# Performance work log

Measured on AMD Instinct MI355X. Metric: run time of the kernel, lower is better.

The kernel has to match this reference:

```python
import jax, jax.numpy as jnp
import numpy as np


def binarize_weight(w):
    # clip to [-1,1], sign in forward, straight-through gradient of clip in backward
    clipped = jnp.clip(w, -1.0, 1.0)
    rounded = jnp.sign(clipped)
    return clipped + jax.lax.stop_gradient(rounded - clipped)


def setup_inputs() -> dict:
    key = jax.random.key(0)
    k1, k2 = jax.random.split(key)
    d_in, filters = 4096, 4096
    n_tokens = 8192
    stdv = 1.0 / np.sqrt(d_in)
    x = jax.random.normal(k1, (n_tokens, d_in), dtype=jnp.float32)
    w = jax.random.normal(k2, (d_in, filters), dtype=jnp.float32) * stdv
    b = jnp.zeros((filters,), dtype=jnp.float32)
    return {"x": x, "w": w, "b": b}


def reference(x, w, b):
    # [N, d_in] @ binarized [d_in, filters] + bias
    out = jnp.matmul(x, binarize_weight(w))
    return out + b
```

## Files before the change

kernel.cpp:

```cpp
#include <hip/hip_runtime.h>
#include <hip/hip_bf16.h>
#include <cstdint>

typedef __attribute__((ext_vector_type(8))) short bf16x8;
typedef __attribute__((ext_vector_type(4))) float f32x4;
typedef __attribute__((ext_vector_type(4))) int   i32x4;
typedef __attribute__((ext_vector_type(16))) int  i32x16;

static constexpr int Mdim = 8192;
static constexpr int Kdim = 4096;
static constexpr int Ndim = 4096;
static constexpr int BM = 256, BN = 256;
static constexpr int BKB = 128;
static constexpr int NKT = Kdim / BKB;

static constexpr int QBLOCKS = Mdim / 4;
static constexpr int SBLOCKS = (Kdim / 64) * (Ndim / 64);

__device__ __forceinline__ void async_copy16(const void* g, void* l) {
  __builtin_amdgcn_global_load_lds(
      (const __attribute__((address_space(1))) void*)g,
      (__attribute__((address_space(3))) void*)l, 16, 0, 0);
}

__global__ __launch_bounds__(256) void prep_kernel(const float* __restrict__ x,
                                                   int8_t* __restrict__ xq,
                                                   float* __restrict__ srow,
                                                   const float* __restrict__ w,
                                                   int8_t* __restrict__ wsT) {
  const int tid = threadIdx.x;
  if (blockIdx.x < QBLOCKS) {
    const int wv  = tid >> 6;
    const int l   = tid & 63;
    const int row = blockIdx.x * 4 + wv;
    const float* xr = x + (size_t)row * Kdim;
    float4 v[16];
    float m = 0.f;
    #pragma unroll
    for (int j = 0; j < 16; ++j) {
      v[j] = *reinterpret_cast<const float4*>(xr + (size_t)(j * 64 + l) * 4);
      m = fmaxf(m, fmaxf(fmaxf(fabsf(v[j].x), fabsf(v[j].y)),
                         fmaxf(fabsf(v[j].z), fabsf(v[j].w))));
    }
    #pragma unroll
    for (int s = 32; s >= 1; s >>= 1) m = fmaxf(m, __shfl_xor(m, s, 64));
    const float rs = (m > 0.f) ? (127.0f / m) : 0.f;
    if (l == 0) srow[row] = m * (1.0f / 127.0f);
    uint32_t* xq32 = reinterpret_cast<uint32_t*>(xq + (size_t)row * Kdim);
    #pragma unroll
    for (int j = 0; j < 16; ++j) {
      int a0 = (int)rintf(v[j].x * rs), a1 = (int)rintf(v[j].y * rs);
      int a2 = (int)rintf(v[j].z * rs), a3 = (int)rintf(v[j].w * rs);
      uint32_t p = (uint32_t)(a0 & 255) | ((uint32_t)(a1 & 255) << 8) |
                   ((uint32_t)(a2 & 255) << 16) | ((uint32_t)(a3 & 255) << 24);
      xq32[j * 64 + l] = p;
    }
  } else {
    __shared__ int8_t t[64 * 68];
    const int bid = blockIdx.x - QBLOCKS;
    const int k0 = (bid & 63) * 64;
    const int n0 = (bid >> 6) * 64;
    #pragma unroll
    for (int r = 0; r < 4; ++r) {
      int c  = r * 256 + tid;
      int k  = c >> 4;
      int n4 = (c & 15) * 4;
      float4 v = *reinterpret_cast<const float4*>(w + (size_t)(k0 + k) * Ndim + n0 + n4);
      int s0 = (v.x > 0.f) - (v.x < 0.f);
      int s1 = (v.y > 0.f) - (v.y < 0.f);
      int s2 = (v.z > 0.f) - (v.z < 0.f);
      int s3 = (v.w > 0.f) - (v.w < 0.f);
      uint32_t p = (uint32_t)(s0 & 255) | ((uint32_t)(s1 & 255) << 8) |
                   ((uint32_t)(s2 & 255) << 16) | ((uint32_t)(s3 & 255) << 24);
      *reinterpret_cast<uint32_t*>(&t[k * 68 + n4]) = p;
    }
    __syncthreads();
    const int n  = tid & 63;
    const int ck = (tid >> 6) * 16;
    union { int8_t b[16]; uint4 u; } o;
    #pragma unroll
    for (int j = 0; j < 16; ++j) o.b[j] = t[(ck + j) * 68 + n];
    *reinterpret_cast<uint4*>(wsT + (size_t)(n0 + n) * Kdim + k0 + ck) = o.u;
  }
}

__global__ __launch_bounds__(512, 2) void gemm_i8_kernel(const int8_t* __restrict__ A,
                                                         const int8_t* __restrict__ Bt,
                                                         const float* __restrict__ srow,
                                                         const float* __restrict__ bias,
                                                         float* __restrict__ out) {
  __shared__ int8_t sA[2][BM * BKB];
  __shared__ int8_t sB[2][BN * BKB];
  const int tid = threadIdx.x;

  const int nwg = (Mdim / BM) * (Ndim / BN);
  const int bid = blockIdx.x;
  const int swz = (bid & 7) * (nwg >> 3) + (bid >> 3);
  const int bm  = swz / (Ndim / BN);
  const int bn  = swz % (Ndim / BN);

  const int lane = tid & 63;
  const int wave = tid >> 6;
  const int wm   = (wave & 1) * 128;
  const int wn   = (wave >> 1) * 64;
  const int m    = lane & 31;
  const int h    = lane >> 5;
  const int em   = m & 7;

  const int8_t* pA[4];
  const int8_t* pB[4];
  #pragma unroll
  for (int p = 0; p < 4; ++p) {
    int s  = tid + 512 * p;
    int r  = s >> 3;
    int cg = (s & 7) ^ (r & 7);
    pA[p] = A  + (size_t)(bm * BM + r) * Kdim + cg * 16;
    pB[p] = Bt + (size_t)(bn * BN + r) * Kdim + cg * 16;
  }

  i32x16 acc[4][2] = {};

  auto stage = [&](int t, int b) {
    const int k0 = t * BKB;
    #pragma unroll
    for (int p = 0; p < 4; ++p) {
      async_copy16(pA[p] + k0, &sA[b][(tid + 512 * p) * 16]);
      async_copy16(pB[p] + k0, &sB[b][(tid + 512 * p) * 16]);
    }
  };

  stage(0, 0);
  asm volatile("" ::: "memory");
  stage(1, 1);

  for (int t = 0; t < NKT; ++t) {
    const int b = t & 1;

    if (t < NKT - 1) asm volatile("s_waitcnt vmcnt(8)" ::: "memory");
    else             asm volatile("s_waitcnt vmcnt(0)" ::: "memory");
    __builtin_amdgcn_sched_barrier(0);
    __builtin_amdgcn_s_barrier();
    __builtin_amdgcn_sched_barrier(0);

    const int8_t* la = &sA[b][0];
    const int8_t* lb = &sB[b][0];
    #pragma unroll
    for (int ks = 0; ks < 4; ++ks) {
      const int cx = ((ks * 2 + h) ^ em) * 16;
      i32x4 af[4], bf[2];
      #pragma unroll
      for (int i = 0; i < 4; ++i)
        af[i] = *reinterpret_cast<const i32x4*>(&la[(wm + i * 32 + m) * BKB + cx]);
      #pragma unroll
      for (int j = 0; j < 2; ++j)
        bf[j] = *reinterpret_cast<const i32x4*>(&lb[(wn + j * 32 + m) * BKB + cx]);
      __builtin_amdgcn_s_setprio(1);
      #pragma unroll
      for (int i = 0; i < 4; ++i)
        #pragma unroll
        for (int j = 0; j < 2; ++j)
          acc[i][j] = __builtin_amdgcn_mfma_i32_32x32x32_i8(af[i], bf[j], acc[i][j], 0, 0, 0);
      __builtin_amdgcn_s_setprio(0);
    }

    __builtin_amdgcn_sched_barrier(0);
    __builtin_amdgcn_s_barrier();
    __builtin_amdgcn_sched_barrier(0);
    if (t < NKT - 2) stage(t + 2, b);
  }

  float bv[2];
  #pragma unroll
  for (int j = 0; j < 2; ++j) bv[j] = bias[bn * BN + wn + j * 32 + m];
  #pragma unroll
  for (int i = 0; i < 4; ++i) {
    const int base_row = bm * BM + wm + i * 32 + 4 * h;
    #pragma unroll
    for (int gg = 0; gg < 4; ++gg) {
      float sv[4];
      #pragma unroll
      for (int rr = 0; rr < 4; ++rr) sv[rr] = srow[base_row + gg * 8 + rr];
      #pragma unroll
      for (int j = 0; j < 2; ++j) {
        const int col = bn * BN + wn + j * 32 + m;
        #pragma unroll
        for (int rr = 0; rr < 4; ++rr) {
          const int reg = gg * 4 + rr;
          out[(size_t)(base_row + gg * 8 + rr) * Ndim + col] =
              (float)acc[i][j][reg] * sv[rr] + bv[j];
        }
      }
    }
  }
}

__global__ __launch_bounds__(256) void gemm_fused_kernel(const float* __restrict__ X,
                                                         const float* __restrict__ W,
                                                         const float* __restrict__ bias,
                                                         float* __restrict__ out) {
  __shared__ __hip_bfloat16 sA[128 * 32];
  __shared__ __hip_bfloat16 sB[128 * 32];
  const int tid  = threadIdx.x;
  const int bn   = blockIdx.x, bm = blockIdx.y;
  const int lane = tid & 63;
  const int wave = tid >> 6;
  const int wm   = (wave & 1) * 64;
  const int wn   = (wave >> 1) * 64;
  const int lr   = lane & 15;
  const int quad = lane >> 4;

  f32x4 acc[4][4] = {};

  for (int k0 = 0; k0 < Kdim; k0 += 32) {
    #pragma unroll
    for (int r = 0; r < 2; ++r) {
      int c = r * 256 + tid;
      int row = c >> 2, col = (c & 3) * 8;
      const float4* p = reinterpret_cast<const float4*>(X + (size_t)(bm * 128 + row) * Kdim + k0 + col);
      float4 v0 = p[0], v1 = p[1];
      float va[8] = {v0.x, v0.y, v0.z, v0.w, v1.x, v1.y, v1.z, v1.w};
      union { __hip_bfloat16 h[8]; uint4 u; } oa;
      #pragma unroll
      for (int u2 = 0; u2 < 8; ++u2) oa.h[u2] = __float2bfloat16(va[u2]);
      *reinterpret_cast<uint4*>(&sA[c * 8]) = oa.u;

      int kl = c >> 4, n8 = (c & 15) * 8;
      const float4* q = reinterpret_cast<const float4*>(W + (size_t)(k0 + kl) * Ndim + bn * 128 + n8);
      float4 w0 = q[0], w1 = q[1];
      float wv[8] = {w0.x, w0.y, w0.z, w0.w, w1.x, w1.y, w1.z, w1.w};
      #pragma unroll
      for (int u2 = 0; u2 < 8; ++u2) {
        float sg = (wv[u2] > 0.f) ? 1.f : ((wv[u2] < 0.f) ? -1.f : 0.f);
        sB[(n8 + u2) * 32 + kl] = __float2bfloat16(sg);
      }
    }
    __syncthreads();

    bf16x8 af[4], bf[4];
    #pragma unroll
    for (int i = 0; i < 4; ++i)
      af[i] = *reinterpret_cast<const bf16x8*>(&sA[(wm + i * 16 + lr) * 32 + quad * 8]);
    #pragma unroll
    for (int j = 0; j < 4; ++j)
      bf[j] = *reinterpret_cast<const bf16x8*>(&sB[(wn + j * 16 + lr) * 32 + quad * 8]);
    #pragma unroll
    for (int i = 0; i < 4; ++i)
      #pragma unroll
      for (int j = 0; j < 4; ++j)
        acc[i][j] = __builtin_amdgcn_mfma_f32_16x16x32_bf16(af[i], bf[j], acc[i][j], 0, 0, 0);
    __syncthreads();
  }

  float bv[4];
  #pragma unroll
  for (int j = 0; j < 4; ++j) bv[j] = bias[bn * 128 + wn + j * 16 + lr];
  #pragma unroll
  for (int i = 0; i < 4; ++i) {
    const size_t rowb = (size_t)(bm * 128 + wm + i * 16 + quad * 4);
    #pragma unroll
    for (int j = 0; j < 4; ++j) {
      const int col = bn * 128 + wn + j * 16 + lr;
      float* o = out + rowb * Ndim + col;
      #pragma unroll
      for (int r = 0; r < 4; ++r)
        o[(size_t)r * Ndim] = acc[i][j][r] + bv[j];
    }
  }
}

extern "C" void kernel_launch(void* const* d_in, const int* in_sizes, int n_in,
                              void* d_out, int out_size, void* d_ws, size_t ws_size,
                              hipStream_t stream) {
  const float* x = (const float*)d_in[0];
  const float* w = (const float*)d_in[1];
  const float* b = (const float*)d_in[2];
  float* out = (float*)d_out;

  const size_t xq_bytes = (size_t)Mdim * Kdim;
  const size_t wt_bytes = (size_t)Ndim * Kdim;
  const size_t sr_bytes = (size_t)Mdim * sizeof(float);
  const size_t need = xq_bytes + wt_bytes + sr_bytes;

  if (ws_size >= need) {
    int8_t* xq  = (int8_t*)d_ws;
    int8_t* wsT = (int8_t*)((char*)d_ws + xq_bytes);
    float* srow = (float*)((char*)d_ws + xq_bytes + wt_bytes);
    prep_kernel<<<QBLOCKS + SBLOCKS, 256, 0, stream>>>(x, xq, srow, w, wsT);
    gemm_i8_kernel<<<(Mdim / BM) * (Ndim / BN), 512, 0, stream>>>(xq, wsT, srow, b, out);
  } else {
    gemm_fused_kernel<<<dim3(Ndim / 128, Mdim / 128), 256, 0, stream>>>(x, w, b, out);
  }
}
```

Before: 426.2 us.

## Use triple-buffered 64-byte K tiles with one barrier per iteration

Halves the K tile to 64 bytes and moves from two LDS buffers to three. The next-next stage is issued right after the first fragment loads, so each iteration needs only one barrier instead of two. The swizzle and wait counts are adjusted to match. This targets barrier stalls and lets global loads overlap MFMA work. In exchange there are twice as many iterations and barriers, and correctness relies on a three-deep ring where the buffer being overwritten was last read an iteration earlier.

```diff
diff --git a/kernel.cpp b/kernel.cpp
--- a/kernel.cpp
+++ b/kernel.cpp
@@ -11,8 +11,9 @@
 static constexpr int Kdim = 4096;
 static constexpr int Ndim = 4096;
 static constexpr int BM = 256, BN = 256;
-static constexpr int BKB = 128;
+static constexpr int BKB = 64;
 static constexpr int NKT = Kdim / BKB;
+static constexpr int TILEB = BM * BKB;
 
 static constexpr int QBLOCKS = Mdim / 4;
 static constexpr int SBLOCKS = (Kdim / 64) * (Ndim / 64);
@@ -89,8 +90,8 @@
                                                          const float* __restrict__ srow,
                                                          const float* __restrict__ bias,
                                                          float* __restrict__ out) {
-  __shared__ int8_t sA[2][BM * BKB];
-  __shared__ int8_t sB[2][BN * BKB];
+  __shared__ int8_t sA[3][TILEB];
+  __shared__ int8_t sB[3][TILEB];
   const int tid = threadIdx.x;
 
   const int nwg = (Mdim / BM) * (Ndim / BN);
@@ -105,27 +106,29 @@
   const int wn   = (wave >> 1) * 64;
   const int m    = lane & 31;
   const int h    = lane >> 5;
-  const int em   = m & 7;
-
-  const int8_t* pA[4];
-  const int8_t* pB[4];
-  #pragma unroll
-  for (int p = 0; p < 4; ++p) {
+  const int em   = m & 3;
+
+  const int8_t* pA[2];
+  const int8_t* pB[2];
+  #pragma unroll
+  for (int p = 0; p < 2; ++p) {
     int s  = tid + 512 * p;
-    int r  = s >> 3;
-    int cg = (s & 7) ^ (r & 7);
+    int r  = s >> 2;
+    int cg = (s & 3) ^ (r & 3);
     pA[p] = A  + (size_t)(bm * BM + r) * Kdim + cg * 16;
     pB[p] = Bt + (size_t)(bn * BN + r) * Kdim + cg * 16;
   }
 
   i32x16 acc[4][2] = {};
 
-  auto stage = [&](int t, int b) {
+  auto stage = [&](int t, int buf) {
     const int k0 = t * BKB;
-    #pragma unroll
-    for (int p = 0; p < 4; ++p) {
-      async_copy16(pA[p] + k0, &sA[b][(tid + 512 * p) * 16]);
-      async_copy16(pB[p] + k0, &sB[b][(tid + 512 * p) * 16]);
+    int8_t* dA = &sA[0][0] + buf * TILEB;
+    int8_t* dB = &sB[0][0] + buf * TILEB;
+    #pragma unroll
+    for (int p = 0; p < 2; ++p) {
+      async_copy16(pA[p] + k0, dA + (tid + 512 * p) * 16);
+      async_copy16(pB[p] + k0, dB + (tid + 512 * p) * 16);
     }
   };
 
@@ -133,40 +136,60 @@
   asm volatile("" ::: "memory");
   stage(1, 1);
 
+  int cur = 0;
   for (int t = 0; t < NKT; ++t) {
-    const int b = t & 1;
-
-    if (t < NKT - 1) asm volatile("s_waitcnt vmcnt(8)" ::: "memory");
+    if (t < NKT - 1) asm volatile("s_waitcnt vmcnt(4)" ::: "memory");
     else             asm volatile("s_waitcnt vmcnt(0)" ::: "memory");
     __builtin_amdgcn_sched_barrier(0);
     __builtin_amdgcn_s_barrier();
     __builtin_amdgcn_sched_barrier(0);
 
-    const int8_t* la = &sA[b][0];
-    const int8_t* lb = &sB[b][0];
-    #pragma unroll
-    for (int ks = 0; ks < 4; ++ks) {
-      const int cx = ((ks * 2 + h) ^ em) * 16;
-      i32x4 af[4], bf[2];
+    const int8_t* la = &sA[0][0] + cur * TILEB;
+    const int8_t* lb = &sB[0][0] + cur * TILEB;
+
+    i32x4 af0[4], bf0[2];
+    {
+      const int cx = (h ^ em) * 16;
       #pragma unroll
       for (int i = 0; i < 4; ++i)
-        af[i] = *reinterpret_cast<const i32x4*>(&la[(wm + i * 32 + m) * BKB + cx]);
+        af0[i] = *reinterpret_cast<const i32x4*>(&la[(wm + i * 32 + m) * BKB + cx]);
       #pragma unroll
       for (int j = 0; j < 2; ++j)
-        bf[j] = *reinterpret_cast<const i32x4*>(&lb[(wn + j * 32 + m) * BKB + cx]);
-      __builtin_amdgcn_s_setprio(1);
+        bf0[j] = *reinterpret_cast<const i32x4*>(&lb[(wn + j * 32 + m) * BKB + cx]);
+    }
+
+    if (t < NKT - 2) {
+      int wb = cur + 2; if (wb >= 3) wb -= 3;
+      stage(t + 2, wb);
+    }
+
+    __builtin_amdgcn_s_setprio(1);
+    #pragma unroll
+    for (int i = 0; i < 4; ++i)
+      #pragma unroll
+      for (int j = 0; j < 2; ++j)
+        acc[i][j] = __builtin_amdgcn_mfma_i32_32x32x32_i8(af0[i], bf0[j], acc[i][j], 0, 0, 0);
+    __builtin_amdgcn_s_setprio(0);
+
+    i32x4 af1[4], bf1[2];
+    {
+      const int cx = ((2 + h) ^ em) * 16;
       #pragma unroll
       for (int i = 0; i < 4; ++i)
-        #pragma unroll
-        for (int j = 0; j < 2; ++j)
-          acc[i][j] = __builtin_amdgcn_mfma_i32_32x32x32_i8(af[i], bf[j], acc[i][j], 0, 0, 0);
-      __builtin_amdgcn_s_setprio(0);
-    }
-
-    __builtin_amdgcn_sched_barrier(0);
-    __builtin_amdgcn_s_barrier();
-    __builtin_amdgcn_sched_barrier(0);
-    if (t < NKT - 2) stage(t + 2, b);
+        af1[i] = *reinterpret_cast<const i32x4*>(&la[(wm + i * 32 + m) * BKB + cx]);
+      #pragma unroll
+      for (int j = 0; j < 2; ++j)
+        bf1[j] = *reinterpret_cast<const i32x4*>(&lb[(wn + j * 32 + m) * BKB + cx]);
+    }
+    __builtin_amdgcn_s_setprio(1);
+    #pragma unroll
+    for (int i = 0; i < 4; ++i)
+      #pragma unroll
+      for (int j = 0; j < 2; ++j)
+        acc[i][j] = __builtin_amdgcn_mfma_i32_32x32x32_i8(af1[i], bf1[j], acc[i][j], 0, 0, 0);
+    __builtin_amdgcn_s_setprio(0);
+
+    cur = (cur + 1 == 3) ? 0 : cur + 1;
   }
 
   float bv[2];
```

Result: slower. 444.3 us (+4.3%).
